# Kernel tuning notes

Measured on AMD Instinct MI355X. Metric: run time of the kernel, lower is better.

## Reference

```python
import jax, jax.numpy as jnp
import numpy as np

B, N, D = 2, 4096, 1024
HID, OUT = 1024, 1
APPERTURE = 256
EPS = 1e-6
Q_SCALE = 0.06


def _ln(x, g, b):
    # torch.std defaults to unbiased (ddof=1); eps added to std, not var
    mean = x.mean(-1, keepdims=True)
    std = jnp.std(x, axis=-1, ddof=1, keepdims=True)
    return g * (x - mean) / (std + EPS) + b


def _self_attn(x, Wk, Wq, Wv, Wo):
    K = x @ Wk.T
    Q = (x @ Wq.T) * Q_SCALE
    V = x @ Wv.T
    logits = jnp.einsum('bnd,bmd->bnm', Q, K)  # [B,N,N]
    idx = jnp.arange(N)
    keep = jnp.abs(idx[:, None] - idx[None, :]) < APPERTURE  # band kept
    logits = jnp.where(keep[None], logits, -jnp.inf)
    w = jax.nn.softmax(logits, axis=-1)
    # torch: y = (V^T @ w)^T  == w^T applied column-wise -> einsum over first attn index
    y = jnp.einsum('bmn,bmd->bnd', w, V)
    return y @ Wo.T


def setup_inputs() -> dict:
    key = jax.random.key(0)
    ks = jax.random.split(key, 20)
    s = 0.02
    inp = {
        'x1': jax.random.normal(ks[0], (B, N, D), jnp.float32),
        'x2': jax.random.normal(ks[1], (B, N, D), jnp.float32),
        'x3': jax.random.normal(ks[2], (B, N, D), jnp.float32),
        'Wk': jax.random.normal(ks[3], (D, D), jnp.float32) * s,
        'Wq': jax.random.normal(ks[4], (D, D), jnp.float32) * s,
        'Wv': jax.random.normal(ks[5], (D, D), jnp.float32) * s,
        'Wo': jax.random.normal(ks[6], (D, D), jnp.float32) * s,
        'ka_w': jax.random.normal(ks[7], (HID, D), jnp.float32) * s,
        'ka_b': jnp.zeros((HID,), jnp.float32),
        'kb_w': jax.random.normal(ks[8], (HID, HID), jnp.float32) * s,
        'kb_b': jnp.zeros((HID,), jnp.float32),
        'kc_w': jax.random.normal(ks[9], (HID, HID), jnp.float32) * s,
        'kc_b': jnp.zeros((HID,), jnp.float32),
        'kd_w': jax.random.normal(ks[10], (OUT, HID), jnp.float32) * s,
        'kd_b': jnp.zeros((OUT,), jnp.float32),
        'g1': jnp.ones((D,), jnp.float32),
        'b1': jnp.zeros((D,), jnp.float32),
        'g2': jnp.ones((HID,), jnp.float32),
        'b2': jnp.zeros((HID,), jnp.float32),
    }
    return inp


def reference(x1, x2, x3, Wk, Wq, Wv, Wo, ka_w, ka_b, kb_w, kb_b,
              kc_w, kc_b, kd_w, kd_b, g1, b1, g2, b2):
    # dropout in eval mode -> identity
    y = jnp.zeros_like(x1)
    for x in (x1, x2, x3):
        a = _self_attn(x, Wk, Wq, Wv, Wo)
        y = y + _ln(a + x, g1, b1)
    y = y @ ka_w.T + ka_b
    y = y @ kb_w.T + kb_b
    y = y @ kc_w.T + kc_b
    y = jax.nn.relu(y)
    y = _ln(y, g2, b2)
    y = y @ kd_w.T + kd_b  # [B,N,1]
    return y.reshape(y.shape[0], -1)  # [B,N]
```

## Files before the change

### kernel.cpp

```cpp
#include <hip/hip_runtime.h>

#define NSEQ 4096
#define DDIM 1024
#define NROWS 8192
#define BAND 512
#define BM 128
#define BN 128
#define BKT 64
#define PT_W 768
#define PT_CH 64

typedef __attribute__((ext_vector_type(8))) __bf16 bf16x8;
typedef __attribute__((ext_vector_type(4))) float f32x4;

__device__ __forceinline__ unsigned short f2b(float f) {
  unsigned int u = __float_as_uint(f);
  unsigned int r = (u + 0x7FFFu + ((u >> 16) & 1u)) >> 16;
  return (unsigned short)r;
}
__device__ __forceinline__ float b2f(unsigned short b) {
  return __uint_as_float(((unsigned int)b) << 16);
}

__device__ __forceinline__ void gload16(const unsigned short* g, unsigned short* l) {
  __builtin_amdgcn_global_load_lds(
      (const __attribute__((address_space(1))) void*)g,
      (__attribute__((address_space(3))) void*)l, 16, 0, 0);
}

__device__ __forceinline__ float blk_sum(float v) {
  __shared__ float red_s[4];
  #pragma unroll
  for (int o = 32; o; o >>= 1) v += __shfl_xor(v, o);
  __syncthreads();
  if ((threadIdx.x & 63) == 0) red_s[threadIdx.x >> 6] = v;
  __syncthreads();
  return red_s[0] + red_s[1] + red_s[2] + red_s[3];
}
__device__ __forceinline__ float blk_max(float v) {
  __shared__ float red_m[4];
  #pragma unroll
  for (int o = 32; o; o >>= 1) v = fmaxf(v, __shfl_xor(v, o));
  __syncthreads();
  if ((threadIdx.x & 63) == 0) red_m[threadIdx.x >> 6] = v;
  __syncthreads();
  return fmaxf(fmaxf(red_m[0], red_m[1]), fmaxf(red_m[2], red_m[3]));
}

__global__ __launch_bounds__(256) void k_cvt(const float* __restrict__ src,
                                             unsigned short* __restrict__ dst,
                                             int n4) {
  int i = blockIdx.x * 256 + threadIdx.x;
  if (i < n4) {
    float4 f = ((const float4*)src)[i];
    ushort4 o = make_ushort4(f2b(f.x), f2b(f.y), f2b(f.z), f2b(f.w));
    ((ushort4*)dst)[i] = o;
  }
}

template<int OMODE>
__global__ __launch_bounds__(256) void k_gemm_bt(
    const unsigned short* __restrict__ A,
    const unsigned short* __restrict__ B,
    void* __restrict__ Cout,
    int K, float alpha, const float* __restrict__ bias, int relu)
{
  __shared__ unsigned short As[BM * BKT];
  __shared__ unsigned short Bs[BN * BKT];
  const int tid = threadIdx.x;
  const int lane = tid & 63, wave = tid >> 6;
  const int wm = wave >> 1, wn = wave & 1;
  const int lrow = lane & 15, kgrp = lane >> 4;
  const int srow = lane >> 3;
  const int sseg = (lane & 7) ^ srow;
  const size_t m0 = (size_t)blockIdx.x * BM;
  const size_t n0 = (size_t)blockIdx.y * BN;
  f32x4 acc[4][4] = {};

  for (int k0 = 0; k0 < K; k0 += BKT) {
    #pragma unroll
    for (int i = 0; i < 4; ++i) {
      int chunk = wave * 4 + i;
      int row = chunk * 8 + srow;
      gload16(A + (m0 + row) * (size_t)K + k0 + sseg * 8, As + chunk * 512);
      gload16(B + (n0 + row) * (size_t)K + k0 + sseg * 8, Bs + chunk * 512);
    }
    __syncthreads();
    #pragma unroll
    for (int ks = 0; ks < 2; ++ks) {
      bf16x8 af[4], bfr[4];
      #pragma unroll
      for (int i = 0; i < 4; ++i)
        af[i] = *(const bf16x8*)&As[(wm * 64 + i * 16 + lrow) * BKT +
                                    (((ks * 4 + kgrp) ^ (lrow & 7)) << 3)];
      #pragma unroll
      for (int j = 0; j < 4; ++j)
        bfr[j] = *(const bf16x8*)&Bs[(wn * 64 + j * 16 + lrow) * BKT +
                                     (((ks * 4 + kgrp) ^ (lrow & 7)) << 3)];
      #pragma unroll
      for (int i = 0; i < 4; ++i)
        #pragma unroll
        for (int j = 0; j < 4; ++j)
          acc[i][j] = __builtin_amdgcn_mfma_f32_16x16x32_bf16(af[i], bfr[j], acc[i][j], 0, 0, 0);
    }
    __syncthreads();
  }

  #pragma unroll
  for (int i = 0; i < 4; ++i) {
    int rbase = (int)m0 + wm * 64 + i * 16 + kgrp * 4;
    #pragma unroll
    for (int j = 0; j < 4; ++j) {
      int col = (int)n0 + wn * 64 + j * 16 + lrow;
      float bv = bias ? bias[col] : 0.f;
      if (OMODE == 2) {
        int b = rbase >> 12, nn = rbase & (NSEQ - 1);
        ushort4 o;
        o.x = f2b(acc[i][j][0] * alpha + bv);
        o.y = f2b(acc[i][j][1] * alpha + bv);
        o.z = f2b(acc[i][j][2] * alpha + bv);
        o.w = f2b(acc[i][j][3] * alpha + bv);
        *(ushort4*)&((unsigned short*)Cout)[((size_t)b * DDIM + col) * NSEQ + nn] = o;
      } else {
        #pragma unroll
        for (int r = 0; r < 4; ++r) {
          int row = rbase + r;
          float v = acc[i][j][r] * alpha + bv;
          if (relu) v = fmaxf(v, 0.f);
          if (OMODE == 0)
            ((float*)Cout)[(size_t)row * DDIM + col] = v;
          else
            ((unsigned short*)Cout)[(size_t)row * DDIM + col] = f2b(v);
        }
      }
    }
  }
}

__global__ __launch_bounds__(256) void k_qk_banded(
    const unsigned short* __restrict__ Q,
    const unsigned short* __restrict__ Kmat,
    float* __restrict__ Sb)
{
  const int m0 = blockIdx.x * BM;
  const int n0 = m0 - 256 + blockIdx.y * BM;
  const int bat = blockIdx.z;
  if (n0 + BM <= 0 || n0 >= NSEQ) return;
  const unsigned short* Ab = Q + (size_t)bat * NSEQ * DDIM;
  const unsigned short* Bb = Kmat + (size_t)bat * NSEQ * DDIM;
  __shared__ unsigned short As[BM * BKT];
  __shared__ unsigned short Bs[BN * BKT];
  const int tid = threadIdx.x;
  const int lane = tid & 63, wave = tid >> 6;
  const int wm = wave >> 1, wn = wave & 1;
  const int lrow = lane & 15, kgrp = lane >> 4;
  const int srow = lane >> 3;
  const int sseg = (lane & 7) ^ srow;
  f32x4 acc[4][4] = {};

  for (int k0 = 0; k0 < DDIM; k0 += BKT) {
    #pragma unroll
    for (int i = 0; i < 4; ++i) {
      int chunk = wave * 4 + i;
      int row = chunk * 8 + srow;
      gload16(Ab + (size_t)(m0 + row) * DDIM + k0 + sseg * 8, As + chunk * 512);
      int nr = n0 + row;
      nr = nr < 0 ? 0 : (nr >= NSEQ ? NSEQ - 1 : nr);
      gload16(Bb + (size_t)nr * DDIM + k0 + sseg * 8, Bs + chunk * 512);
    }
    __syncthreads();
    #pragma unroll
    for (int ks = 0; ks < 2; ++ks) {
      bf16x8 af[4], bfr[4];
      #pragma unroll
      for (int i = 0; i < 4; ++i)
        af[i] = *(const bf16x8*)&As[(wm * 64 + i * 16 + lrow) * BKT +
                                    (((ks * 4 + kgrp) ^ (lrow & 7)) << 3)];
      #pragma unroll
      for (int j = 0; j < 4; ++j)
        bfr[j] = *(const bf16x8*)&Bs[(wn * 64 + j * 16 + lrow) * BKT +
                                     (((ks * 4 + kgrp) ^ (lrow & 7)) << 3)];
      #pragma unroll
      for (int i = 0; i < 4; ++i)
        #pragma unroll
        for (int j = 0; j < 4; ++j)
          acc[i][j] = __builtin_amdgcn_mfma_f32_16x16x32_bf16(af[i], bfr[j], acc[i][j], 0, 0, 0);
    }
    __syncthreads();
  }

  #pragma unroll
  for (int i = 0; i < 4; ++i) {
    #pragma unroll
    for (int j = 0; j < 4; ++j) {
      int n = n0 + wn * 64 + j * 16 + lrow;
      #pragma unroll
      for (int r = 0; r < 4; ++r) {
        int m = m0 + wm * 64 + i * 16 + kgrp * 4 + r;
        int dlt = n - m;
        if (n >= 0 && n < NSEQ && dlt >= -255 && dlt <= 255)
          Sb[((size_t)bat * NSEQ + m) * BAND + (dlt + 255)] = acc[i][j][r];
      }
    }
  }
}

__global__ __launch_bounds__(256) void k_softmax(
    const float* __restrict__ Sb, unsigned short* __restrict__ Pb)
{
  int row = blockIdx.x;
  int m = row & (NSEQ - 1);
  int tid = threadIdx.x;
  int jlo = max(0, 255 - m);
  int jhi = min(510, NSEQ - 1 - m + 255);
  const float* S = Sb + (size_t)row * BAND;
  int j0 = tid, j1 = tid + 256;
  bool ok0 = (j0 >= jlo) && (j0 <= jhi);
  bool ok1 = (j1 >= jlo) && (j1 <= jhi);
  float v0 = ok0 ? S[j0] : -1e30f;
  float v1 = ok1 ? S[j1] : -1e30f;
  float mx = blk_max(fmaxf(v0, v1));
  float e0 = ok0 ? __expf(v0 - mx) : 0.f;
  float e1 = ok1 ? __expf(v1 - mx) : 0.f;
  float sum = blk_sum(e0 + e1);
  float inv = 1.f / sum;
  unsigned short* P = Pb + (size_t)row * BAND;
  P[j0] = f2b(e0 * inv);
  P[j1] = f2b(e1 * inv);
}

__global__ __launch_bounds__(256) void k_transpose(
    const unsigned short* __restrict__ Pb, unsigned short* __restrict__ Pt)
{
  const int c = blockIdx.x;
  const int s = blockIdx.y;
  const int bat = blockIdx.z;
  const unsigned short* Pbb = Pb + (size_t)bat * NSEQ * BAND;
  unsigned short* Ptb = Pt + ((size_t)bat * PT_CH + c) * PT_W * 64;
  __shared__ unsigned short Ts[64][130];
  const int t = threadIdx.x;
  const int half = t >> 7;
  const int jl = t & 127;
  #pragma unroll
  for (int e = 0; e < 32; ++e) {
    int mp = e * 2 + half;
    int j = s * 128 + jl - mp - 65;
    unsigned short v = 0;
    if (j >= 0 && j < BAND) v = Pbb[(size_t)(c * 64 + mp) * BAND + j];
    Ts[mp][jl] = v;
  }
  __syncthreads();
  const int nl = t >> 1;
  const int mg = t & 1;
  unsigned short* orow = Ptb + (size_t)(s * 128 + nl) * 64;
  #pragma unroll
  for (int v4 = 0; v4 < 4; ++v4) {
    int lc = mg * 4 + v4;
    int sc = lc ^ (nl & 7);
    __align__(16) unsigned short tmp[8];
    #pragma unroll
    for (int i = 0; i < 8; ++i) tmp[i] = Ts[lc * 8 + i][nl];
    *(uint4*)(orow + sc * 8) = *(const uint4*)tmp;
  }
}

__global__ __launch_bounds__(256) void k_pv(
    const unsigned short* __restrict__ Pt,
    const unsigned short* __restrict__ Vt,
    unsigned short* __restrict__ Y)
{
  const int n0 = blockIdx.x * BM;
  const int d0 = blockIdx.y * BN;
  const int bat = blockIdx.z;
  const int tid = threadIdx.x;
  const int lane = tid & 63, wave = tid >> 6;
  const int wm = wave >> 1, wn = wave & 1;
  const int lrow = lane & 15, kgrp = lane >> 4;
  const int srow = lane >> 3;
  const int sseg = (lane & 7) ^ srow;
  __shared__ unsigned short As[BM * BKT];
  __shared__ unsigned short Bs[BN * BKT];
  f32x4 acc[4][4] = {};
  const unsigned short* Ptb = Pt + (size_t)bat * PT_CH * PT_W * 64;
  const unsigned short* Vtb = Vt + (size_t)bat * DDIM * NSEQ;

  for (int kk = 0; kk < 10; ++kk) {
    int mb = n0 - 256 + kk * 64;
    if (mb < 0 || mb >= NSEQ) continue;
    int c = mb >> 6;
    int np0 = 576 - kk * 64;
    const unsigned short* Abase = Ptb + ((size_t)c * PT_W + np0) * 64;
    #pragma unroll
    for (int i = 0; i < 4; ++i) {
      int chunk = wave * 4 + i;
      int row = chunk * 8 + srow;
      gload16(Abase + chunk * 512 + (size_t)lane * 8, As + chunk * 512);
      gload16(Vtb + (size_t)(d0 + row) * NSEQ + mb + sseg * 8, Bs + chunk * 512);
    }
    __syncthreads();
    #pragma unroll
    for (int ks = 0; ks < 2; ++ks) {
      bf16x8 af[4], bfr[4];
      #pragma unroll
      for (int i = 0; i < 4; ++i)
        af[i] = *(const bf16x8*)&As[(wm * 64 + i * 16 + lrow) * BKT +
                                    (((ks * 4 + kgrp) ^ (lrow & 7)) << 3)];
      #pragma unroll
      for (int j = 0; j < 4; ++j)
        bfr[j] = *(const bf16x8*)&Bs[(wn * 64 + j * 16 + lrow) * BKT +
                                     (((ks * 4 + kgrp) ^ (lrow & 7)) << 3)];
      #pragma unroll
      for (int i = 0; i < 4; ++i)
        #pragma unroll
        for (int j = 0; j < 4; ++j)
          acc[i][j] = __builtin_amdgcn_mfma_f32_16x16x32_bf16(af[i], bfr[j], acc[i][j], 0, 0, 0);
    }
    __syncthreads();
  }

  unsigned short* Yb = Y + (size_t)bat * NSEQ * DDIM;
  #pragma unroll
  for (int i = 0; i < 4; ++i) {
    int nb = n0 + wm * 64 + i * 16 + kgrp * 4;
    #pragma unroll
    for (int j = 0; j < 4; ++j) {
      int d = d0 + wn * 64 + j * 16 + lrow;
      #pragma unroll
      for (int r = 0; r < 4; ++r)
        Yb[(size_t)(nb + r) * DDIM + d] = f2b(acc[i][j][r]);
    }
  }
}

__global__ __launch_bounds__(256) void k_ln_add(
    const unsigned short* __restrict__ Araw, const float* __restrict__ X,
    const float* __restrict__ g, const float* __restrict__ bb,
    float* __restrict__ Ys, int accum)
{
  int row = blockIdx.x;
  int tid = threadIdx.x;
  const unsigned short* a = Araw + (size_t)row * DDIM;
  const float* x = X + (size_t)row * DDIM;
  ushort4 a4 = ((const ushort4*)a)[tid];
  float4 x4 = ((const float4*)x)[tid];
  float v[4];
  v[0] = b2f(a4.x) + x4.x;
  v[1] = b2f(a4.y) + x4.y;
  v[2] = b2f(a4.z) + x4.z;
  v[3] = b2f(a4.w) + x4.w;
  float s = v[0] + v[1] + v[2] + v[3];
  float mu = blk_sum(s) * (1.f / DDIM);
  float q = 0.f;
  #pragma unroll
  for (int i = 0; i < 4; ++i) { float d = v[i] - mu; q += d * d; }
  float var = blk_sum(q) * (1.f / (DDIM - 1));
  float inv = 1.f / (sqrtf(var) + 1e-6f);
  float4 g4 = ((const float4*)g)[tid];
  float4 b4 = ((const float4*)bb)[tid];
  float* y = Ys + (size_t)row * DDIM;
  float4 o;
  o.x = g4.x * (v[0] - mu) * inv + b4.x;
  o.y = g4.y * (v[1] - mu) * inv + b4.y;
  o.z = g4.z * (v[2] - mu) * inv + b4.z;
  o.w = g4.w * (v[3] - mu) * inv + b4.w;
  if (accum) {
    float4 prev = ((const float4*)y)[tid];
    o.x += prev.x; o.y += prev.y; o.z += prev.z; o.w += prev.w;
  }
  ((float4*)y)[tid] = o;
}

__global__ __launch_bounds__(256) void k_ln_dot(
    const unsigned short* __restrict__ H,
    const float* __restrict__ g, const float* __restrict__ bb,
    const float* __restrict__ kw, const float* __restrict__ kb,
    float* __restrict__ out)
{
  int row = blockIdx.x;
  int tid = threadIdx.x;
  const unsigned short* h = H + (size_t)row * DDIM;
  ushort4 h4 = ((const ushort4*)h)[tid];
  float v[4] = {b2f(h4.x), b2f(h4.y), b2f(h4.z), b2f(h4.w)};
  float s = v[0] + v[1] + v[2] + v[3];
  float mu = blk_sum(s) * (1.f / DDIM);
  float q = 0.f;
  #pragma unroll
  for (int i = 0; i < 4; ++i) { float d = v[i] - mu; q += d * d; }
  float var = blk_sum(q) * (1.f / (DDIM - 1));
  float inv = 1.f / (sqrtf(var) + 1e-6f);
  float4 g4 = ((const float4*)g)[tid];
  float4 b4 = ((const float4*)bb)[tid];
  float4 k4 = ((const float4*)kw)[tid];
  float p = (g4.x * (v[0] - mu) * inv + b4.x) * k4.x
          + (g4.y * (v[1] - mu) * inv + b4.y) * k4.y
          + (g4.z * (v[2] - mu) * inv + b4.z) * k4.z
          + (g4.w * (v[3] - mu) * inv + b4.w) * k4.w;
  float tot = blk_sum(p);
  if (tid == 0) out[row] = tot + kb[0];
}

extern "C" void kernel_launch(void* const* d_in, const int* in_sizes, int n_in,
                              void* d_out, int out_size, void* d_ws, size_t ws_size,
                              hipStream_t stream)
{
  const float* xin[3] = {(const float*)d_in[0], (const float*)d_in[1], (const float*)d_in[2]};
  const float* Wk = (const float*)d_in[3];
  const float* Wq = (const float*)d_in[4];
  const float* Wv = (const float*)d_in[5];
  const float* Wo = (const float*)d_in[6];
  const float* ka_w = (const float*)d_in[7];
  const float* ka_b = (const float*)d_in[8];
  const float* kb_w = (const float*)d_in[9];
  const float* kb_b = (const float*)d_in[10];
  const float* kc_w = (const float*)d_in[11];
  const float* kc_b = (const float*)d_in[12];
  const float* kd_w = (const float*)d_in[13];
  const float* kd_b = (const float*)d_in[14];
  const float* g1 = (const float*)d_in[15];
  const float* b1 = (const float*)d_in[16];
  const float* g2 = (const float*)d_in[17];
  const float* b2 = (const float*)d_in[18];

  const size_t MB = 1024ull * 1024ull;
  char* base = (char*)d_ws;
  unsigned short* WkB = (unsigned short*)(base + 0 * MB);
  unsigned short* WqB = (unsigned short*)(base + 2 * MB);
  unsigned short* WvB = (unsigned short*)(base + 4 * MB);
  unsigned short* WoB = (unsigned short*)(base + 6 * MB);
  unsigned short* kaB = (unsigned short*)(base + 8 * MB);
  unsigned short* kbB = (unsigned short*)(base + 10 * MB);
  unsigned short* kcB = (unsigned short*)(base + 12 * MB);
  char* p = base + 14 * MB;
  unsigned short* xB = (unsigned short*)p;
  unsigned short* aB = (unsigned short*)p;
  p += 32 * MB;
  unsigned short* Qb = (unsigned short*)p;
  unsigned short* Pb = (unsigned short*)p;
  unsigned short* h2 = (unsigned short*)p;
  p += 16 * MB;
  unsigned short* Kb = (unsigned short*)p;
  unsigned short* Ya = (unsigned short*)p;
  unsigned short* h3 = (unsigned short*)p;
  p += 16 * MB;
  unsigned short* VtB = (unsigned short*)p; p += 16 * MB;
  float* Sb = (float*)p;
  unsigned short* PtB = (unsigned short*)p;
  p += 16 * MB;
  float* ysum = (float*)p; p += 32 * MB;
  unsigned short* yB = (unsigned short*)p; p += 16 * MB;
  unsigned short* h1 = (unsigned short*)p; p += 16 * MB;
  (void)ws_size; (void)in_sizes; (void)n_in; (void)out_size;

  dim3 blk(256);
  const int W4 = (DDIM * DDIM) / 4;
  k_cvt<<<1024, blk, 0, stream>>>(Wk, WkB, W4);
  k_cvt<<<1024, blk, 0, stream>>>(Wq, WqB, W4);
  k_cvt<<<1024, blk, 0, stream>>>(Wv, WvB, W4);
  k_cvt<<<1024, blk, 0, stream>>>(Wo, WoB, W4);
  k_cvt<<<1024, blk, 0, stream>>>(ka_w, kaB, W4);
  k_cvt<<<1024, blk, 0, stream>>>(kb_w, kbB, W4);
  k_cvt<<<1024, blk, 0, stream>>>(kc_w, kcB, W4);

  dim3 ggemm(NROWS / BM, DDIM / BN, 1);
  const int X4 = (NROWS * DDIM) / 4;

  for (int br = 0; br < 3; ++br) {
    k_cvt<<<8192, blk, 0, stream>>>(xin[br], xB, X4);
    k_gemm_bt<1><<<ggemm, blk, 0, stream>>>(xB, WkB, Kb, DDIM, 1.f, nullptr, 0);
    k_gemm_bt<1><<<ggemm, blk, 0, stream>>>(xB, WqB, Qb, DDIM, 0.06f, nullptr, 0);
    k_gemm_bt<2><<<ggemm, blk, 0, stream>>>(xB, WvB, VtB, DDIM, 1.f, nullptr, 0);
    k_qk_banded<<<dim3(NSEQ / BM, 5, 2), blk, 0, stream>>>(Qb, Kb, Sb);
    k_softmax<<<NROWS, blk, 0, stream>>>(Sb, Pb);
    k_transpose<<<dim3(PT_CH, PT_W / 128, 2), blk, 0, stream>>>(Pb, PtB);
    k_pv<<<dim3(NSEQ / BM, DDIM / BN, 2), blk, 0, stream>>>(PtB, VtB, Ya);
    k_gemm_bt<1><<<ggemm, blk, 0, stream>>>(Ya, WoB, aB, DDIM, 1.f, nullptr, 0);
    k_ln_add<<<NROWS, blk, 0, stream>>>(aB, xin[br], g1, b1, ysum, br);
  }

  k_cvt<<<8192, blk, 0, stream>>>(ysum, yB, X4);
  k_gemm_bt<1><<<ggemm, blk, 0, stream>>>(yB, kaB, h1, DDIM, 1.f, ka_b, 0);
  k_gemm_bt<1><<<ggemm, blk, 0, stream>>>(h1, kbB, h2, DDIM, 1.f, kb_b, 0);
  k_gemm_bt<1><<<ggemm, blk, 0, stream>>>(h2, kcB, h3, DDIM, 1.f, kc_b, 1);
  k_ln_dot<<<NROWS, blk, 0, stream>>>(h3, g2, b2, kd_w, kd_b, (float*)d_out);
}
```

Baseline: 867.8 us.

## Batch three attention branches into single launches and fuse QKV projection GEMM

Processes all three input branches together by stacking them along the batch dimension, so each attention stage runs as one launch over 6 batch slices instead of three sequential launches. Q, K and V projections are fused into one GEMM against a concatenated 3072-wide weight matrix, with per-segment epilogues that scale Q and transpose V. The three layernorm-add passes are merged into one kernel that writes the bf16 sum directly, which removes the fp32 accumulation buffer and its separate conversion. Larger grids aim to fill the GPU better and cut launch and memory traffic, at the cost of a larger workspace and more aliasing of buffers.

```diff
diff --git a/kernel.cpp b/kernel.cpp
--- a/kernel.cpp
+++ b/kernel.cpp
@@ -3,6 +3,7 @@
 #define NSEQ 4096
 #define DDIM 1024
 #define NROWS 8192
+#define NROWS3 24576
 #define BAND 512
 #define BM 128
 #define BN 128
@@ -58,12 +59,13 @@
   }
 }
 
-template<int OMODE>
-__global__ __launch_bounds__(256) void k_gemm_bt(
+
+__global__ __launch_bounds__(256) void k_gemm_qkv(
     const unsigned short* __restrict__ A,
-    const unsigned short* __restrict__ B,
-    void* __restrict__ Cout,
-    int K, float alpha, const float* __restrict__ bias, int relu)
+    const unsigned short* __restrict__ W,
+    unsigned short* __restrict__ Kout,
+    unsigned short* __restrict__ Qout,
+    unsigned short* __restrict__ Vtout)
 {
   __shared__ unsigned short As[BM * BKT];
   __shared__ unsigned short Bs[BN * BKT];
@@ -77,13 +79,13 @@
   const size_t n0 = (size_t)blockIdx.y * BN;
   f32x4 acc[4][4] = {};
 
-  for (int k0 = 0; k0 < K; k0 += BKT) {
+  for (int k0 = 0; k0 < DDIM; k0 += BKT) {
     #pragma unroll
     for (int i = 0; i < 4; ++i) {
       int chunk = wave * 4 + i;
       int row = chunk * 8 + srow;
-      gload16(A + (m0 + row) * (size_t)K + k0 + sseg * 8, As + chunk * 512);
-      gload16(B + (n0 + row) * (size_t)K + k0 + sseg * 8, Bs + chunk * 512);
+      gload16(A + (m0 + row) * (size_t)DDIM + k0 + sseg * 8, As + chunk * 512);
+      gload16(W + (n0 + row) * (size_t)DDIM + k0 + sseg * 8, Bs + chunk * 512);
     }
     __syncthreads();
     #pragma unroll
@@ -106,6 +108,80 @@
     __syncthreads();
   }
 
+  const int seg = (int)(n0 >> 10);
+  const float al = (seg == 1) ? 0.06f : 1.f;
+  #pragma unroll
+  for (int i = 0; i < 4; ++i) {
+    int rbase = (int)m0 + wm * 64 + i * 16 + kgrp * 4;
+    #pragma unroll
+    for (int j = 0; j < 4; ++j) {
+      int col = (int)n0 + wn * 64 + j * 16 + lrow;
+      int d = col & 1023;
+      if (seg == 2) {
+        int z = rbase >> 12, nn = rbase & (NSEQ - 1);
+        ushort4 o;
+        o.x = f2b(acc[i][j][0]);
+        o.y = f2b(acc[i][j][1]);
+        o.z = f2b(acc[i][j][2]);
+        o.w = f2b(acc[i][j][3]);
+        *(ushort4*)&Vtout[((size_t)z * DDIM + d) * NSEQ + nn] = o;
+      } else {
+        unsigned short* dst = (seg == 1 ? Qout : Kout);
+        #pragma unroll
+        for (int r = 0; r < 4; ++r)
+          dst[(size_t)(rbase + r) * DDIM + d] = f2b(acc[i][j][r] * al);
+      }
+    }
+  }
+}
+
+__global__ __launch_bounds__(256) void k_gemm_bt(
+    const unsigned short* __restrict__ A,
+    const unsigned short* __restrict__ B,
+    unsigned short* __restrict__ Cout,
+    const float* __restrict__ bias, int relu)
+{
+  __shared__ unsigned short As[BM * BKT];
+  __shared__ unsigned short Bs[BN * BKT];
+  const int tid = threadIdx.x;
+  const int lane = tid & 63, wave = tid >> 6;
+  const int wm = wave >> 1, wn = wave & 1;
+  const int lrow = lane & 15, kgrp = lane >> 4;
+  const int srow = lane >> 3;
+  const int sseg = (lane & 7) ^ srow;
+  const size_t m0 = (size_t)blockIdx.x * BM;
+  const size_t n0 = (size_t)blockIdx.y * BN;
+  f32x4 acc[4][4] = {};
+
+  for (int k0 = 0; k0 < DDIM; k0 += BKT) {
+    #pragma unroll
+    for (int i = 0; i < 4; ++i) {
+      int chunk = wave * 4 + i;
+      int row = chunk * 8 + srow;
+      gload16(A + (m0 + row) * (size_t)DDIM + k0 + sseg * 8, As + chunk * 512);
+      gload16(B + (n0 + row) * (size_t)DDIM + k0 + sseg * 8, Bs + chunk * 512);
+    }
+    __syncthreads();
+    #pragma unroll
+    for (int ks = 0; ks < 2; ++ks) {
+      bf16x8 af[4], bfr[4];
+      #pragma unroll
+      for (int i = 0; i < 4; ++i)
+        af[i] = *(const bf16x8*)&As[(wm * 64 + i * 16 + lrow) * BKT +
+                                    (((ks * 4 + kgrp) ^ (lrow & 7)) << 3)];
+      #pragma unroll
+      for (int j = 0; j < 4; ++j)
+        bfr[j] = *(const bf16x8*)&Bs[(wn * 64 + j * 16 + lrow) * BKT +
+                                     (((ks * 4 + kgrp) ^ (lrow & 7)) << 3)];
+      #pragma unroll
+      for (int i = 0; i < 4; ++i)
+        #pragma unroll
+        for (int j = 0; j < 4; ++j)
+          acc[i][j] = __builtin_amdgcn_mfma_f32_16x16x32_bf16(af[i], bfr[j], acc[i][j], 0, 0, 0);
+    }
+    __syncthreads();
+  }
+
   #pragma unroll
   for (int i = 0; i < 4; ++i) {
     int rbase = (int)m0 + wm * 64 + i * 16 + kgrp * 4;
@@ -113,25 +189,11 @@
     for (int j = 0; j < 4; ++j) {
       int col = (int)n0 + wn * 64 + j * 16 + lrow;
       float bv = bias ? bias[col] : 0.f;
-      if (OMODE == 2) {
-        int b = rbase >> 12, nn = rbase & (NSEQ - 1);
-        ushort4 o;
-        o.x = f2b(acc[i][j][0] * alpha + bv);
-        o.y = f2b(acc[i][j][1] * alpha + bv);
-        o.z = f2b(acc[i][j][2] * alpha + bv);
-        o.w = f2b(acc[i][j][3] * alpha + bv);
-        *(ushort4*)&((unsigned short*)Cout)[((size_t)b * DDIM + col) * NSEQ + nn] = o;
-      } else {
-        #pragma unroll
-        for (int r = 0; r < 4; ++r) {
-          int row = rbase + r;
-          float v = acc[i][j][r] * alpha + bv;
-          if (relu) v = fmaxf(v, 0.f);
-          if (OMODE == 0)
-            ((float*)Cout)[(size_t)row * DDIM + col] = v;
-          else
-            ((unsigned short*)Cout)[(size_t)row * DDIM + col] = f2b(v);
-        }
+      #pragma unroll
+      for (int r = 0; r < 4; ++r) {
+        float v = acc[i][j][r] + bv;
+        if (relu) v = fmaxf(v, 0.f);
+        Cout[(size_t)(rbase + r) * DDIM + col] = f2b(v);
       }
     }
   }
@@ -144,10 +206,10 @@
 {
   const int m0 = blockIdx.x * BM;
   const int n0 = m0 - 256 + blockIdx.y * BM;
-  const int bat = blockIdx.z;
+  const int z = blockIdx.z;
   if (n0 + BM <= 0 || n0 >= NSEQ) return;
-  const unsigned short* Ab = Q + (size_t)bat * NSEQ * DDIM;
-  const unsigned short* Bb = Kmat + (size_t)bat * NSEQ * DDIM;
+  const unsigned short* Ab = Q + (size_t)z * NSEQ * DDIM;
+  const unsigned short* Bb = Kmat + (size_t)z * NSEQ * DDIM;
   __shared__ unsigned short As[BM * BKT];
   __shared__ unsigned short Bs[BN * BKT];
   const int tid = threadIdx.x;
@@ -189,6 +251,7 @@
     __syncthreads();
   }
 
+  float* Sz = Sb + (size_t)z * NSEQ * BAND;
   #pragma unroll
   for (int i = 0; i < 4; ++i) {
     #pragma unroll
@@ -199,7 +262,7 @@
         int m = m0 + wm * 64 + i * 16 + kgrp * 4 + r;
         int dlt = n - m;
         if (n >= 0 && n < NSEQ && dlt >= -255 && dlt <= 255)
-          Sb[((size_t)bat * NSEQ + m) * BAND + (dlt + 255)] = acc[i][j][r];
+          Sz[(size_t)m * BAND + (dlt + 255)] = acc[i][j][r];
       }
     }
   }
@@ -234,9 +297,9 @@
 {
   const int c = blockIdx.x;
   const int s = blockIdx.y;
-  const int bat = blockIdx.z;
-  const unsigned short* Pbb = Pb + (size_t)bat * NSEQ * BAND;
-  unsigned short* Ptb = Pt + ((size_t)bat * PT_CH + c) * PT_W * 64;
+  const int z = blockIdx.z;
+  const unsigned short* Pbb = Pb + (size_t)z * NSEQ * BAND;
+  unsigned short* Ptb = Pt + ((size_t)z * PT_CH + c) * PT_W * 64;
   __shared__ unsigned short Ts[64][130];
   const int t = threadIdx.x;
   const int half = t >> 7;
@@ -271,7 +334,7 @@
 {
   const int n0 = blockIdx.x * BM;
   const int d0 = blockIdx.y * BN;
-  const int bat = blockIdx.z;
+  const int z = blockIdx.z;
   const int tid = threadIdx.x;
   const int lane = tid & 63, wave = tid >> 6;
   const int wm = wave >> 1, wn = wave & 1;
@@ -281,8 +344,8 @@
   __shared__ unsigned short As[BM * BKT];
   __shared__ unsigned short Bs[BN * BKT];
   f32x4 acc[4][4] = {};
-  const unsigned short* Ptb = Pt + (size_t)bat * PT_CH * PT_W * 64;
-  const unsigned short* Vtb = Vt + (size_t)bat * DDIM * NSEQ;
+  const unsigned short* Ptb = Pt + (size_t)z * PT_CH * PT_W * 64;
+  const unsigned short* Vtb = Vt + (size_t)z * DDIM * NSEQ;
 
   for (int kk = 0; kk < 10; ++kk) {
     int mb = n0 - 256 + kk * 64;
@@ -318,7 +381,7 @@
     __syncthreads();
   }
 
-  unsigned short* Yb = Y + (size_t)bat * NSEQ * DDIM;
+  unsigned short* Yb = Y + (size_t)z * NSEQ * DDIM;
   #pragma unroll
   for (int i = 0; i < 4; ++i) {
     int nb = n0 + wm * 64 + i * 16 + kgrp * 4;
@@ -332,42 +395,43 @@
   }
 }
 
-__global__ __launch_bounds__(256) void k_ln_add(
-    const unsigned short* __restrict__ Araw, const float* __restrict__ X,
+__global__ __launch_bounds__(256) void k_ln3(
+    const unsigned short* __restrict__ aB,
+    const float* __restrict__ x1, const float* __restrict__ x2,
+    const float* __restrict__ x3,
     const float* __restrict__ g, const float* __restrict__ bb,
-    float* __restrict__ Ys, int accum)
+    unsigned short* __restrict__ yB)
 {
   int row = blockIdx.x;
   int tid = threadIdx.x;
-  const unsigned short* a = Araw + (size_t)row * DDIM;
-  const float* x = X + (size_t)row * DDIM;
-  ushort4 a4 = ((const ushort4*)a)[tid];
-  float4 x4 = ((const float4*)x)[tid];
-  float v[4];
-  v[0] = b2f(a4.x) + x4.x;
-  v[1] = b2f(a4.y) + x4.y;
-  v[2] = b2f(a4.z) + x4.z;
-  v[3] = b2f(a4.w) + x4.w;
-  float s = v[0] + v[1] + v[2] + v[3];
-  float mu = blk_sum(s) * (1.f / DDIM);
-  float q = 0.f;
-  #pragma unroll
-  for (int i = 0; i < 4; ++i) { float d = v[i] - mu; q += d * d; }
-  float var = blk_sum(q) * (1.f / (DDIM - 1));
-  float inv = 1.f / (sqrtf(var) + 1e-6f);
+  const float* xs[3] = {x1, x2, x3};
+  float o[4] = {0.f, 0.f, 0.f, 0.f};
   float4 g4 = ((const float4*)g)[tid];
   float4 b4 = ((const float4*)bb)[tid];
-  float* y = Ys + (size_t)row * DDIM;
-  float4 o;
-  o.x = g4.x * (v[0] - mu) * inv + b4.x;
-  o.y = g4.y * (v[1] - mu) * inv + b4.y;
-  o.z = g4.z * (v[2] - mu) * inv + b4.z;
-  o.w = g4.w * (v[3] - mu) * inv + b4.w;
-  if (accum) {
-    float4 prev = ((const float4*)y)[tid];
-    o.x += prev.x; o.y += prev.y; o.z += prev.z; o.w += prev.w;
-  }
-  ((float4*)y)[tid] = o;
+  #pragma unroll
+  for (int br = 0; br < 3; ++br) {
+    const unsigned short* a = aB + (size_t)(br * NROWS + row) * DDIM;
+    const float* x = xs[br] + (size_t)row * DDIM;
+    ushort4 a4 = ((const ushort4*)a)[tid];
+    float4 x4 = ((const float4*)x)[tid];
+    float v[4];
+    v[0] = b2f(a4.x) + x4.x;
+    v[1] = b2f(a4.y) + x4.y;
+    v[2] = b2f(a4.z) + x4.z;
+    v[3] = b2f(a4.w) + x4.w;
+    float mu = blk_sum(v[0] + v[1] + v[2] + v[3]) * (1.f / DDIM);
+    float q = 0.f;
+    #pragma unroll
+    for (int i = 0; i < 4; ++i) { float d = v[i] - mu; q += d * d; }
+    float var = blk_sum(q) * (1.f / (DDIM - 1));
+    float inv = 1.f / (sqrtf(var) + 1e-6f);
+    o[0] += g4.x * (v[0] - mu) * inv + b4.x;
+    o[1] += g4.y * (v[1] - mu) * inv + b4.y;
+    o[2] += g4.z * (v[2] - mu) * inv + b4.z;
+    o[3] += g4.w * (v[3] - mu) * inv + b4.w;
+  }
+  ushort4 w = make_ushort4(f2b(o[0]), f2b(o[1]), f2b(o[2]), f2b(o[3]));
+  ((ushort4*)(yB + (size_t)row * DDIM))[tid] = w;
 }
 
 __global__ __launch_bounds__(256) void k_ln_dot(
@@ -381,8 +445,7 @@
   const unsigned short* h = H + (size_t)row * DDIM;
   ushort4 h4 = ((const ushort4*)h)[tid];
   float v[4] = {b2f(h4.x), b2f(h4.y), b2f(h4.z), b2f(h4.w)};
-  float s = v[0] + v[1] + v[2] + v[3];
-  float mu = blk_sum(s) * (1.f / DDIM);
+  float mu = blk_sum(v[0] + v[1] + v[2] + v[3]) * (1.f / DDIM);
   float q = 0.f;
   #pragma unroll
   for (int i = 0; i < 4; ++i) { float d = v[i] - mu; q += d * d; }
@@ -403,7 +466,9 @@
                               void* d_out, int out_size, void* d_ws, size_t ws_size,
                               hipStream_t stream)
 {
-  const float* xin[3] = {(const float*)d_in[0], (const float*)d_in[1], (const float*)d_in[2]};
+  const float* x1 = (const float*)d_in[0];
+  const float* x2 = (const float*)d_in[1];
+  const float* x3 = (const float*)d_in[2];
   const float* Wk = (const float*)d_in[3];
   const float* Wq = (const float*)d_in[4];
   const float* Wv = (const float*)d_in[5];
@@ -424,62 +489,50 @@
   const size_t MB = 1024ull * 1024ull;
   char* base = (char*)d_ws;
   unsigned short* WkB = (unsigned short*)(base + 0 * MB);
-  unsigned short* WqB = (unsigned short*)(base + 2 * MB);
-  unsigned short* WvB = (unsigned short*)(base + 4 * MB);
   unsigned short* WoB = (unsigned short*)(base + 6 * MB);
   unsigned short* kaB = (unsigned short*)(base + 8 * MB);
   unsigned short* kbB = (unsigned short*)(base + 10 * MB);
   unsigned short* kcB = (unsigned short*)(base + 12 * MB);
-  char* p = base + 14 * MB;
-  unsigned short* xB = (unsigned short*)p;
-  unsigned short* aB = (unsigned short*)p;
-  p += 32 * MB;
-  unsigned short* Qb = (unsigned short*)p;
-  unsigned short* Pb = (unsigned short*)p;
-  unsigned short* h2 = (unsigned short*)p;
-  p += 16 * MB;
-  unsigned short* Kb = (unsigned short*)p;
-  unsigned short* Ya = (unsigned short*)p;
-  unsigned short* h3 = (unsigned short*)p;
-  p += 16 * MB;
-  unsigned short* VtB = (unsigned short*)p; p += 16 * MB;
-  float* Sb = (float*)p;
-  unsigned short* PtB = (unsigned short*)p;
-  p += 16 * MB;
-  float* ysum = (float*)p; p += 32 * MB;
-  unsigned short* yB = (unsigned short*)p; p += 16 * MB;
-  unsigned short* h1 = (unsigned short*)p; p += 16 * MB;
+  unsigned short* xB = (unsigned short*)(base + 14 * MB);
+  float* Sb = (float*)(base + 14 * MB);
+  unsigned short* aB = (unsigned short*)(base + 14 * MB);
+  unsigned short* Kb = (unsigned short*)(base + 62 * MB);
+  unsigned short* Pb = (unsigned short*)(base + 62 * MB);
+  unsigned short* Ya = (unsigned short*)(base + 62 * MB);
+  unsigned short* Qb = (unsigned short*)(base + 110 * MB);
+  unsigned short* PtB = (unsigned short*)(base + 110 * MB);
+  unsigned short* yB = (unsigned short*)(base + 110 * MB);
+  unsigned short* h1 = (unsigned short*)(base + 126 * MB);
+  unsigned short* h2 = (unsigned short*)(base + 142 * MB);
+  unsigned short* VtB = (unsigned short*)(base + 158 * MB);
+  unsigned short* h3 = (unsigned short*)(base + 158 * MB);
   (void)ws_size; (void)in_sizes; (void)n_in; (void)out_size;
 
   dim3 blk(256);
   const int W4 = (DDIM * DDIM) / 4;
   k_cvt<<<1024, blk, 0, stream>>>(Wk, WkB, W4);
-  k_cvt<<<1024, blk, 0, stream>>>(Wq, WqB, W4);
-  k_cvt<<<1024, blk, 0, stream>>>(Wv, WvB, W4);
+  k_cvt<<<1024, blk, 0, stream>>>(Wq, WkB + 1024 * 1024, W4);
+  k_cvt<<<1024, blk, 0, stream>>>(Wv, WkB + 2 * 1024 * 1024, W4);
   k_cvt<<<1024, blk, 0, stream>>>(Wo, WoB, W4);
   k_cvt<<<1024, blk, 0, stream>>>(ka_w, kaB, W4);
   k_cvt<<<1024, blk, 0, stream>>>(kb_w, kbB, W4);
   k_cvt<<<1024, blk, 0, stream>>>(kc_w, kcB, W4);
 
-  dim3 ggemm(NROWS / BM, DDIM / BN, 1);
   const int X4 = (NROWS * DDIM) / 4;
-
-  for (int br = 0; br < 3; ++br) {
-    k_cvt<<<8192, blk, 0, stream>>>(xin[br], xB, X4);
-    k_gemm_bt<1><<<ggemm, blk, 0, stream>>>(xB, WkB, Kb, DDIM, 1.f, nullptr, 0);
-    k_gemm_bt<1><<<ggemm, blk, 0, stream>>>(xB, WqB, Qb, DDIM, 0.06f, nullptr, 0);
-    k_gemm_bt<2><<<ggemm, blk, 0, stream>>>(xB, WvB, VtB, DDIM, 1.f, nullptr, 0);
-    k_qk_banded<<<dim3(NSEQ / BM, 5, 2), blk, 0, stream>>>(Qb, Kb, Sb);
-    k_softmax<<<NROWS, blk, 0, stream>>>(Sb, Pb);
-    k_transpose<<<dim3(PT_CH, PT_W / 128, 2), blk, 0, stream>>>(Pb, PtB);
-    k_pv<<<dim3(NSEQ / BM, DDIM / BN, 2), blk, 0, stream>>>(PtB, VtB, Ya);
-    k_gemm_bt<1><<<ggemm, blk, 0, stream>>>(Ya, WoB, aB, DDIM, 1.f, nullptr, 0);
-    k_ln_add<<<NROWS, blk, 0, stream>>>(aB, xin[br], g1, b1, ysum, br);
-  }
-
-  k_cvt<<<8192, blk, 0, stream>>>(ysum, yB, X4);
-  k_gemm_bt<1><<<ggemm, blk, 0, stream>>>(yB, kaB, h1, DDIM, 1.f, ka_b, 0);
-  k_gemm_bt<1><<<ggemm, blk, 0, stream>>>(h1, kbB, h2, DDIM, 1.f, kb_b, 0);
-  k_gemm_bt<1><<<ggemm, blk, 0, stream>>>(h2, kcB, h3, DDIM, 1.f, kc_b, 1);
+  k_cvt<<<8192, blk, 0, stream>>>(x1, xB, X4);
+  k_cvt<<<8192, blk, 0, stream>>>(x2, xB + (size_t)NROWS * DDIM, X4);
+  k_cvt<<<8192, blk, 0, stream>>>(x3, xB + 2 * (size_t)NROWS * DDIM, X4);
+
+  k_gemm_qkv<<<dim3(NROWS3 / BM, 3072 / BN), blk, 0, stream>>>(xB, WkB, Kb, Qb, VtB);
+  k_qk_banded<<<dim3(NSEQ / BM, 5, 6), blk, 0, stream>>>(Qb, Kb, Sb);
+  k_softmax<<<NROWS3, blk, 0, stream>>>(Sb, Pb);
+  k_transpose<<<dim3(PT_CH, PT_W / 128, 6), blk, 0, stream>>>(Pb, PtB);
+  k_pv<<<dim3(NSEQ / BM, DDIM / BN, 6), blk, 0, stream>>>(PtB, VtB, Ya);
+  k_gemm_bt<<<dim3(NROWS3 / BM, DDIM / BN), blk, 0, stream>>>(Ya, WoB, aB, nullptr, 0);
+  k_ln3<<<NROWS, blk, 0, stream>>>(aB, x1, x2, x3, g1, b1, yB);
+  dim3 gm(NROWS / BM, DDIM / BN);
+  k_gemm_bt<<<gm, blk, 0, stream>>>(yB, kaB, h1, ka_b, 0);
+  k_gemm_bt<<<gm, blk, 0, stream>>>(h1, kbB, h2, kb_b, 0);
+  k_gemm_bt<<<gm, blk, 0, stream>>>(h2, kcB, h3, kc_b, 1);
   k_ln_dot<<<NROWS, blk, 0, stream>>>(h3, g2, b2, kd_w, kd_b, (float*)d_out);
 }
```

Result: faster. 782.8 us (-9.8%).
